# Kernel tuning notes

Measured on AMD Instinct MI355X. Metric: run time of the kernel, lower is better.

The kernel has to match this reference:

```python
import jax, jax.numpy as jnp
import numpy as np

D = 1024  # input_dim


def setup_inputs() -> dict:
    key = jax.random.key(0)
    ks = jax.random.split(key, 7)
    scale = 1.0 / np.sqrt(D)
    x = jax.random.normal(ks[0], (4, D, 2048), dtype=jnp.float32)
    Wq = jax.random.uniform(ks[1], (D, D), jnp.float32, -scale, scale)
    bq = jax.random.uniform(ks[2], (D,), jnp.float32, -scale, scale)
    Wk = jax.random.uniform(ks[3], (D, D), jnp.float32, -scale, scale)
    bk = jax.random.uniform(ks[4], (D,), jnp.float32, -scale, scale)
    Wv = jax.random.uniform(ks[5], (D, D), jnp.float32, -scale, scale)
    bv = jax.random.uniform(ks[6], (D,), jnp.float32, -scale, scale)
    return {"x": x, "Wq": Wq, "bq": bq, "Wk": Wk, "bk": bk, "Wv": Wv, "bv": bv}


def reference(x, Wq, bq, Wk, bk, Wv, bv):
    # x: [B, D, S] -> [B, S, D]
    xt = jnp.transpose(x, (0, 2, 1))
    # torch nn.Linear: y = x @ W^T + b
    q = jnp.einsum('bsd,ed->bse', xt, Wq) + bq
    k = jnp.einsum('bsd,ed->bse', xt, Wk) + bk
    v = jnp.einsum('bsd,ed->bse', xt, Wv) + bv
    scores = jnp.einsum('bse,bte->bst', q, k) / jnp.sqrt(jnp.float32(D))
    attn = jax.nn.softmax(scores, axis=2)
    out = jnp.einsum('bst,bte->bse', attn, v)  # [B, S, D]
    return out
```

## Files before the change

### kernel.cpp

```cpp
#include <hip/hip_runtime.h>
#include <stdint.h>

typedef unsigned short us16;
typedef unsigned short us8  __attribute__((ext_vector_type(8)));
typedef unsigned short us4v __attribute__((ext_vector_type(4)));
typedef __bf16         bf16x8 __attribute__((ext_vector_type(8)));
typedef float          f32x4  __attribute__((ext_vector_type(4)));

__device__ __forceinline__ us16 f2bf(float f) {
    union { float f; unsigned int u; } c; c.f = f;
    unsigned int u = (c.u + 0x7fffu + ((c.u >> 16) & 1u)) >> 16;
    return (us16)u;
}
__device__ __forceinline__ float bf2f(us16 h) {
    union { unsigned int u; float f; } c; c.u = ((unsigned int)h) << 16;
    return c.f;
}

__device__ __forceinline__ void async16(const us16* g, us16* l) {
    __builtin_amdgcn_global_load_lds(
        (const __attribute__((address_space(1))) unsigned int*)g,
        (__attribute__((address_space(3))) unsigned int*)l,
        16, 0, 0);
}

template <int EPI>
__device__ __forceinline__ void gemm_core(
        const us16* __restrict__ A, const us16* __restrict__ B,
        void* __restrict__ C, const float* __restrict__ bias,
        float* __restrict__ L,
        int M, int K, int x, int y, us16* lsA, us16* lsB) {
    const int m0 = x * 128, n0 = y * 128;
    const int tid = threadIdx.x;
    const int lane = tid & 63, wid = tid >> 6;
    const int l15 = lane & 15, quad = lane >> 4;
    const int wm = (wid & 1) * 64, wn = (wid >> 1) * 64;

    f32x4 acc[4][4] = {};

    const int srow = wid * 32 + (lane >> 3);
    const int sc8 = (lane & 7) ^ ((lane >> 3) & 7);
    const us16* Ap = A + (size_t)(m0 + srow) * K + sc8 * 8;
    const us16* Bp = B + (size_t)(n0 + srow) * K + sc8 * 8;
    us16* ldsAw = &lsA[(wid * 32) * 64];
    us16* ldsBw = &lsB[(wid * 32) * 64];

    for (int kb = 0; kb < K; kb += 64) {
        __syncthreads();
#pragma unroll
        for (int c = 0; c < 4; c++) {
            async16(Ap + kb + (size_t)(c * 8) * K, ldsAw + c * 8 * 64);
            async16(Bp + kb + (size_t)(c * 8) * K, ldsBw + c * 8 * 64);
        }
        __syncthreads();
#pragma unroll
        for (int ks = 0; ks < 2; ks++) {
            bf16x8 af[4], bfr[4];
#pragma unroll
            for (int i = 0; i < 4; i++) {
                const int ra = wm + i * 16 + l15;
                const int rb = wn + i * 16 + l15;
                const int pa = ((ks * 4 + quad) ^ (ra & 7)) * 8;
                const int pb = ((ks * 4 + quad) ^ (rb & 7)) * 8;
                af[i]  = *(const bf16x8*)(&lsA[ra * 64 + pa]);
                bfr[i] = *(const bf16x8*)(&lsB[rb * 64 + pb]);
            }
#pragma unroll
            for (int i = 0; i < 4; i++)
#pragma unroll
                for (int j = 0; j < 4; j++)
                    acc[i][j] = __builtin_amdgcn_mfma_f32_16x16x32_bf16(af[i], bfr[j], acc[i][j], 0, 0, 0);
        }
    }

    if (EPI == 2) {
        const float scale = 0.03125f;
        float rs[4] = {0.f, 0.f, 0.f, 0.f};
#pragma unroll
        for (int i = 0; i < 4; i++) {
            const int mb = m0 + wm + i * 16 + quad * 4;
#pragma unroll
            for (int j = 0; j < 4; j++) {
                const int n = n0 + wn + j * 16 + l15;
                f32x4 v = acc[i][j];
                const float e0 = __expf(v[0] * scale), e1 = __expf(v[1] * scale);
                const float e2 = __expf(v[2] * scale), e3 = __expf(v[3] * scale);
                rs[j] += (e0 + e1) + (e2 + e3);
                us4v st = { f2bf(e0), f2bf(e1), f2bf(e2), f2bf(e3) };
                *(us4v*)((us16*)C + (size_t)n * M + mb) = st;
            }
        }
#pragma unroll
        for (int j = 0; j < 4; j++) {
            rs[j] += __shfl_xor(rs[j], 16, 64);
            rs[j] += __shfl_xor(rs[j], 32, 64);
        }
        if (quad == 0) {
#pragma unroll
            for (int j = 0; j < 4; j++)
                atomicAdd(&L[n0 + wn + j * 16 + l15], rs[j]);
        }
        return;
    }

#pragma unroll
    for (int i = 0; i < 4; i++) {
        const int mb = m0 + wm + i * 16 + quad * 4;
        float b0 = 0.f, b1 = 0.f, b2 = 0.f, b3 = 0.f;
        if (EPI == 0) {
            float4 bv4 = *(const float4*)(bias + mb);
            b0 = bv4.x; b1 = bv4.y; b2 = bv4.z; b3 = bv4.w;
        }
#pragma unroll
        for (int j = 0; j < 4; j++) {
            const int n = n0 + wn + j * 16 + l15;
            f32x4 v = acc[i][j];
            if (EPI == 3) {
                const float inv = 1.0f / L[n];
                float4 st;
                st.x = v[0] * inv; st.y = v[1] * inv;
                st.z = v[2] * inv; st.w = v[3] * inv;
                *(float4*)((float*)C + (size_t)n * M + mb) = st;
            } else {
                const float bn = (EPI == 1) ? bias[n] : 0.0f;
                us4v st = { f2bf(v[0] + b0 + bn), f2bf(v[1] + b1 + bn),
                            f2bf(v[2] + b2 + bn), f2bf(v[3] + b3 + bn) };
                *(us4v*)((us16*)C + (size_t)n * M + mb) = st;
            }
        }
    }
}

__device__ __forceinline__ void strip_xy(int lin, int gy, int& x, int& y) {
    const int within = lin & (4 * gy - 1);
    x = (lin / (4 * gy)) * 4 + (within & 3);
    y = within >> 2;
}

__global__ __launch_bounds__(256)
void prep(const float* __restrict__ x, us16* __restrict__ xt,
          const float* __restrict__ wq, const float* __restrict__ wk,
          const float* __restrict__ wv, us16* __restrict__ wb) {
    __shared__ us16 tile[64 * 65];
    const int id = blockIdx.x;
    const int t = threadIdx.x;
    if (id < 2048) {
        const int s0 = (id & 31) * 64, d0 = ((id >> 5) & 15) * 64, b = id >> 9;
        const float* xp = x + ((size_t)b * 1024 + d0) * 2048 + s0;
        const int r = t >> 4, c4 = t & 15;
#pragma unroll
        for (int i = 0; i < 4; i++) {
            float4 v = *(const float4*)(xp + (size_t)(r + 16 * i) * 2048 + c4 * 4);
            const int d = r + 16 * i;
            tile[(c4 * 4 + 0) * 65 + d] = f2bf(v.x);
            tile[(c4 * 4 + 1) * 65 + d] = f2bf(v.y);
            tile[(c4 * 4 + 2) * 65 + d] = f2bf(v.z);
            tile[(c4 * 4 + 3) * 65 + d] = f2bf(v.w);
        }
        __syncthreads();
        us16* op = xt + ((size_t)b * 2048 + s0) * 1024 + d0;
#pragma unroll
        for (int i = 0; i < 2; i++) {
            const int u = t + 256 * i;
            const int s = u >> 3, c8 = u & 7;
            us8 o;
#pragma unroll
            for (int j = 0; j < 8; j++) o[j] = tile[s * 65 + c8 * 8 + j];
            *(us8*)(op + (size_t)s * 1024 + c8 * 8) = o;
        }
    } else {
        const int cid = id - 2048;
        const int mb = cid >> 10;
        const float* src = (mb == 0) ? wq : (mb == 1) ? wk : wv;
        const size_t off = ((size_t)(cid & 1023) * 256 + t) * 4;
        float4 v = *(const float4*)(src + off);
        us4v o = { f2bf(v.x), f2bf(v.y), f2bf(v.z), f2bf(v.w) };
        *(us4v*)(wb + (size_t)mb * 1048576 + off) = o;
    }
}

__global__ __launch_bounds__(256)
void qkv(const us16* __restrict__ Wb, const us16* __restrict__ XT,
         us16* __restrict__ Qb, us16* __restrict__ Kb, us16* __restrict__ VT,
         const float* __restrict__ bq, const float* __restrict__ bk,
         const float* __restrict__ bv) {
    __shared__ us16 lsA[128 * 64];
    __shared__ us16 lsB[128 * 64];
    const int id = blockIdx.x;
    const long long sXT = 2097152;
    if (id < 1024) {
        const int z = id >> 7, zz = z & 3;
        const bool isK = z >= 4;
        int x, y; strip_xy(id & 127, 16, x, y);
        const us16* A = Wb + (isK ? 1048576 : 0);
        const us16* B = XT + (size_t)zz * sXT;
        us16* C = (isK ? Kb : Qb) + (size_t)zz * sXT;
        gemm_core<0>(A, B, (void*)C, isK ? bk : bq, nullptr, 1024, 1024, x, y, lsA, lsB);
    } else {
        const int id2 = id - 1024;
        const int z = id2 >> 7;
        int x, y; strip_xy(id2 & 127, 8, x, y);
        const us16* A = XT + (size_t)z * sXT;
        us16* C = VT + (size_t)z * sXT;
        gemm_core<1>(A, Wb + 2097152, (void*)C, bv, nullptr, 2048, 1024, x, y, lsA, lsB);
    }
}

__global__ __launch_bounds__(256)
void scores_k(const us16* __restrict__ Kb, const us16* __restrict__ Qb,
              us16* __restrict__ Sb, float* __restrict__ L) {
    __shared__ us16 lsA[128 * 64];
    __shared__ us16 lsB[128 * 64];
    const long long sXT = 2097152, sSS = 4194304;
    const int z = blockIdx.z;
    int x, y; strip_xy(blockIdx.x + 16 * blockIdx.y, 16, x, y);
    gemm_core<2>(Kb + (size_t)z * sXT, Qb + (size_t)z * sXT,
                 (void*)(Sb + (size_t)z * sSS), nullptr, L + z * 2048,
                 2048, 1024, x, y, lsA, lsB);
}

__global__ __launch_bounds__(256)
void out_k(const us16* __restrict__ VT, const us16* __restrict__ Sb,
           float* __restrict__ L, float* __restrict__ out) {
    __shared__ us16 lsA[128 * 64];
    __shared__ us16 lsB[128 * 64];
    const long long sXT = 2097152, sSS = 4194304;
    const int z = blockIdx.z;
    int x, y; strip_xy(blockIdx.x + 8 * blockIdx.y, 16, x, y);
    gemm_core<3>(VT + (size_t)z * sXT, Sb + (size_t)z * sSS,
                 (void*)(out + (size_t)z * sXT), nullptr, L + z * 2048,
                 1024, 2048, x, y, lsA, lsB);
}

extern "C" void kernel_launch(void* const* d_in, const int* in_sizes, int n_in,
                              void* d_out, int out_size, void* d_ws, size_t ws_size,
                              hipStream_t stream) {
    const float* x  = (const float*)d_in[0];
    const float* Wq = (const float*)d_in[1];
    const float* bq = (const float*)d_in[2];
    const float* Wk = (const float*)d_in[3];
    const float* bk = (const float*)d_in[4];
    const float* Wv = (const float*)d_in[5];
    const float* bv = (const float*)d_in[6];
    float* out = (float*)d_out;
    char* ws = (char*)d_ws;

    const size_t SZ = 16777216;
    us16* Qb = (us16*)(ws);
    us16* Kb = (us16*)(ws + SZ);
    us16* VT = (us16*)(ws + 2 * SZ);
    us16* XT = (us16*)(ws + 3 * SZ);
    us16* Wb = (us16*)(ws + 4 * SZ);
    us16* Sb = (us16*)(ws + 3 * SZ);
    float* Lb = (float*)(ws + 5 * SZ);

    dim3 blk(256, 1, 1);

    hipMemsetAsync(Lb, 0, 4 * 2048 * sizeof(float), stream);
    prep<<<dim3(5120, 1, 1), blk, 0, stream>>>(x, XT, Wq, Wk, Wv, Wb);
    qkv<<<dim3(1536, 1, 1), blk, 0, stream>>>(Wb, XT, Qb, Kb, VT, bq, bk, bv);
    scores_k<<<dim3(16, 16, 4), blk, 0, stream>>>(Kb, Qb, Sb, Lb);
    out_k<<<dim3(8, 16, 4), blk, 0, stream>>>(VT, Sb, Lb, out);
}
```

Measured before the change: 252.4 us.

## Replace GEMM core with 4-stage async pipelined, larger-tile 512-thread kernel

Replaces the synchronous load-then-compute GEMM loop with a 4-buffer software pipeline that prefetches three K-slices of 32 ahead using async global-to-LDS loads. The code waits on them with explicit vmcnt counts and a single barrier per step. Tiles grow to 256x256 or 128x256 with 8 waves per block, and MFMA sections get raised priority. The aim is to hide global memory latency and increase reuse per block. The cost is much larger LDS use and fewer blocks, so occupancy and tail balance are at risk.

```diff
diff --git a/kernel.cpp b/kernel.cpp
--- a/kernel.cpp
+++ b/kernel.cpp
@@ -12,10 +12,6 @@
     unsigned int u = (c.u + 0x7fffu + ((c.u >> 16) & 1u)) >> 16;
     return (us16)u;
 }
-__device__ __forceinline__ float bf2f(us16 h) {
-    union { unsigned int u; float f; } c; c.u = ((unsigned int)h) << 16;
-    return c.f;
-}
 
 __device__ __forceinline__ void async16(const us16* g, us16* l) {
     __builtin_amdgcn_global_load_lds(
@@ -24,64 +20,113 @@
         16, 0, 0);
 }
 
-template <int EPI>
-__device__ __forceinline__ void gemm_core(
+template <int N> __device__ __forceinline__ void wait_vm() {
+    if constexpr (N == 8)      asm volatile("s_waitcnt vmcnt(8)" ::: "memory");
+    else if constexpr (N == 6) asm volatile("s_waitcnt vmcnt(6)" ::: "memory");
+    else if constexpr (N == 4) asm volatile("s_waitcnt vmcnt(4)" ::: "memory");
+    else if constexpr (N == 3) asm volatile("s_waitcnt vmcnt(3)" ::: "memory");
+    else                       asm volatile("s_waitcnt vmcnt(0)" ::: "memory");
+}
+
+template <int EPI, int MI, int NJ>
+__device__ __forceinline__ void gemm_pipe(
         const us16* __restrict__ A, const us16* __restrict__ B,
         void* __restrict__ C, const float* __restrict__ bias,
         float* __restrict__ L,
-        int M, int K, int x, int y, us16* lsA, us16* lsB) {
-    const int m0 = x * 128, n0 = y * 128;
-    const int tid = threadIdx.x;
+        int M, int K, int x, int y, us16* lds) {
+    constexpr int BM  = 32 * MI;
+    constexpr int BN  = 64 * NJ;
+    constexpr int IA  = BM / 128;
+    constexpr int IB  = BN / 128;
+    constexpr int EA  = BM * 32;
+    constexpr int BUF = EA + BN * 32;
+    constexpr int LD  = IA + IB;
+
+    const int tid  = threadIdx.x;
     const int lane = tid & 63, wid = tid >> 6;
-    const int l15 = lane & 15, quad = lane >> 4;
-    const int wm = (wid & 1) * 64, wn = (wid >> 1) * 64;
-
-    f32x4 acc[4][4] = {};
-
-    const int srow = wid * 32 + (lane >> 3);
-    const int sc8 = (lane & 7) ^ ((lane >> 3) & 7);
-    const us16* Ap = A + (size_t)(m0 + srow) * K + sc8 * 8;
-    const us16* Bp = B + (size_t)(n0 + srow) * K + sc8 * 8;
-    us16* ldsAw = &lsA[(wid * 32) * 64];
-    us16* ldsBw = &lsB[(wid * 32) * 64];
-
-    for (int kb = 0; kb < K; kb += 64) {
-        __syncthreads();
-#pragma unroll
-        for (int c = 0; c < 4; c++) {
-            async16(Ap + kb + (size_t)(c * 8) * K, ldsAw + c * 8 * 64);
-            async16(Bp + kb + (size_t)(c * 8) * K, ldsBw + c * 8 * 64);
-        }
-        __syncthreads();
-#pragma unroll
-        for (int ks = 0; ks < 2; ks++) {
-            bf16x8 af[4], bfr[4];
-#pragma unroll
-            for (int i = 0; i < 4; i++) {
-                const int ra = wm + i * 16 + l15;
-                const int rb = wn + i * 16 + l15;
-                const int pa = ((ks * 4 + quad) ^ (ra & 7)) * 8;
-                const int pb = ((ks * 4 + quad) ^ (rb & 7)) * 8;
-                af[i]  = *(const bf16x8*)(&lsA[ra * 64 + pa]);
-                bfr[i] = *(const bf16x8*)(&lsB[rb * 64 + pb]);
-            }
-#pragma unroll
-            for (int i = 0; i < 4; i++)
-#pragma unroll
-                for (int j = 0; j < 4; j++)
-                    acc[i][j] = __builtin_amdgcn_mfma_f32_16x16x32_bf16(af[i], bfr[j], acc[i][j], 0, 0, 0);
-        }
+    const int l15  = lane & 15, quad = lane >> 4;
+    const int wm   = wid >> 2, wn = wid & 3;
+    const int m0   = x * BM, n0 = y * BN;
+
+    const int gc8  = (((lane & 3) ^ ((lane >> 2) & 3) ^ ((lane >> 4) & 3))) * 8;
+    const int lsub = lane >> 2;
+
+    const us16* Ag[IA]; int Al[IA];
+#pragma unroll
+    for (int c = 0; c < IA; c++) {
+        const int r = wid * (16 * IA) + c * 16;
+        Ag[c] = A + (size_t)(m0 + r + lsub) * K + gc8;
+        Al[c] = r * 32;
+    }
+    const us16* Bg[IB]; int Bl[IB];
+#pragma unroll
+    for (int c = 0; c < IB; c++) {
+        const int r = wid * (16 * IB) + c * 16;
+        Bg[c] = B + (size_t)(n0 + r + lsub) * K + gc8;
+        Bl[c] = EA + r * 32;
+    }
+
+    const int NT  = K >> 5;
+    const int rc8    = ((quad ^ (l15 & 3) ^ ((l15 >> 2) & 3))) * 8;
+    const int raBase = wm * (MI * 16) + l15;
+    const int rbBase = wn * (NJ * 16) + l15;
+
+    f32x4 acc[MI][NJ] = {};
+
+#pragma unroll
+    for (int t = 0; t < 3; t++) {
+        us16* bp = lds + t * BUF;
+        const int ko = t * 32;
+#pragma unroll
+        for (int c = 0; c < IA; c++) async16(Ag[c] + ko, bp + Al[c]);
+#pragma unroll
+        for (int c = 0; c < IB; c++) async16(Bg[c] + ko, bp + Bl[c]);
+    }
+    wait_vm<2 * LD>();
+    __builtin_amdgcn_s_barrier();
+
+    for (int t = 0; t < NT; t++) {
+        if (t + 3 < NT) {
+            us16* bp = lds + ((t + 3) & 3) * BUF;
+            const int ko = (t + 3) * 32;
+#pragma unroll
+            for (int c = 0; c < IA; c++) async16(Ag[c] + ko, bp + Al[c]);
+#pragma unroll
+            for (int c = 0; c < IB; c++) async16(Bg[c] + ko, bp + Bl[c]);
+        }
+        const us16* bp = lds + (t & 3) * BUF;
+        bf16x8 af[MI], bfv[NJ];
+#pragma unroll
+        for (int i = 0; i < MI; i++)
+            af[i]  = *(const bf16x8*)(bp + (raBase + i * 16) * 32 + rc8);
+#pragma unroll
+        for (int j = 0; j < NJ; j++)
+            bfv[j] = *(const bf16x8*)(bp + EA + (rbBase + j * 16) * 32 + rc8);
+        __builtin_amdgcn_s_setprio(1);
+#pragma unroll
+        for (int i = 0; i < MI; i++)
+#pragma unroll
+            for (int j = 0; j < NJ; j++)
+                acc[i][j] = __builtin_amdgcn_mfma_f32_16x16x32_bf16(af[i], bfv[j], acc[i][j], 0, 0, 0);
+        __builtin_amdgcn_s_setprio(0);
+        if (t + 3 < NT)      wait_vm<2 * LD>();
+        else if (t + 2 < NT) wait_vm<LD>();
+        else if (t + 1 < NT) wait_vm<0>();
+        __builtin_amdgcn_sched_barrier(0);
+        __builtin_amdgcn_s_barrier();
     }
 
     if (EPI == 2) {
         const float scale = 0.03125f;
-        float rs[4] = {0.f, 0.f, 0.f, 0.f};
-#pragma unroll
-        for (int i = 0; i < 4; i++) {
-            const int mb = m0 + wm + i * 16 + quad * 4;
-#pragma unroll
-            for (int j = 0; j < 4; j++) {
-                const int n = n0 + wn + j * 16 + l15;
+        float rs[NJ];
+#pragma unroll
+        for (int j = 0; j < NJ; j++) rs[j] = 0.f;
+#pragma unroll
+        for (int i = 0; i < MI; i++) {
+            const int mb = m0 + wm * (MI * 16) + i * 16 + quad * 4;
+#pragma unroll
+            for (int j = 0; j < NJ; j++) {
+                const int n = n0 + wn * (NJ * 16) + j * 16 + l15;
                 f32x4 v = acc[i][j];
                 const float e0 = __expf(v[0] * scale), e1 = __expf(v[1] * scale);
                 const float e2 = __expf(v[2] * scale), e3 = __expf(v[3] * scale);
@@ -91,29 +136,29 @@
             }
         }
 #pragma unroll
-        for (int j = 0; j < 4; j++) {
+        for (int j = 0; j < NJ; j++) {
             rs[j] += __shfl_xor(rs[j], 16, 64);
             rs[j] += __shfl_xor(rs[j], 32, 64);
         }
         if (quad == 0) {
 #pragma unroll
-            for (int j = 0; j < 4; j++)
-                atomicAdd(&L[n0 + wn + j * 16 + l15], rs[j]);
+            for (int j = 0; j < NJ; j++)
+                atomicAdd(&L[n0 + wn * (NJ * 16) + j * 16 + l15], rs[j]);
         }
         return;
     }
 
 #pragma unroll
-    for (int i = 0; i < 4; i++) {
-        const int mb = m0 + wm + i * 16 + quad * 4;
+    for (int i = 0; i < MI; i++) {
+        const int mb = m0 + wm * (MI * 16) + i * 16 + quad * 4;
         float b0 = 0.f, b1 = 0.f, b2 = 0.f, b3 = 0.f;
         if (EPI == 0) {
             float4 bv4 = *(const float4*)(bias + mb);
             b0 = bv4.x; b1 = bv4.y; b2 = bv4.z; b3 = bv4.w;
         }
 #pragma unroll
-        for (int j = 0; j < 4; j++) {
-            const int n = n0 + wn + j * 16 + l15;
+        for (int j = 0; j < NJ; j++) {
+            const int n = n0 + wn * (NJ * 16) + j * 16 + l15;
             f32x4 v = acc[i][j];
             if (EPI == 3) {
                 const float inv = 1.0f / L[n];
@@ -179,57 +224,55 @@
     }
 }
 
-__global__ __launch_bounds__(256)
+__global__ __launch_bounds__(512)
 void qkv(const us16* __restrict__ Wb, const us16* __restrict__ XT,
          us16* __restrict__ Qb, us16* __restrict__ Kb, us16* __restrict__ VT,
          const float* __restrict__ bq, const float* __restrict__ bk,
          const float* __restrict__ bv) {
-    __shared__ us16 lsA[128 * 64];
-    __shared__ us16 lsB[128 * 64];
+    __shared__ __align__(16) us16 lds[65536];
     const int id = blockIdx.x;
     const long long sXT = 2097152;
-    if (id < 1024) {
-        const int z = id >> 7, zz = z & 3;
+    if (id < 256) {
+        const int z = id >> 5, zz = z & 3;
         const bool isK = z >= 4;
-        int x, y; strip_xy(id & 127, 16, x, y);
+        int x, y; strip_xy(id & 31, 8, x, y);
         const us16* A = Wb + (isK ? 1048576 : 0);
         const us16* B = XT + (size_t)zz * sXT;
         us16* C = (isK ? Kb : Qb) + (size_t)zz * sXT;
-        gemm_core<0>(A, B, (void*)C, isK ? bk : bq, nullptr, 1024, 1024, x, y, lsA, lsB);
+        gemm_pipe<0, 8, 4>(A, B, (void*)C, isK ? bk : bq, nullptr,
+                           1024, 1024, x, y, lds);
     } else {
-        const int id2 = id - 1024;
-        const int z = id2 >> 7;
-        int x, y; strip_xy(id2 & 127, 8, x, y);
-        const us16* A = XT + (size_t)z * sXT;
-        us16* C = VT + (size_t)z * sXT;
-        gemm_core<1>(A, Wb + 2097152, (void*)C, bv, nullptr, 2048, 1024, x, y, lsA, lsB);
-    }
-}
-
-__global__ __launch_bounds__(256)
+        const int id2 = id - 256;
+        const int z = id2 >> 6;
+        int x, y; strip_xy(id2 & 63, 4, x, y);
+        gemm_pipe<1, 4, 4>(XT + (size_t)z * sXT, Wb + 2097152,
+                           (void*)(VT + (size_t)z * sXT), bv, nullptr,
+                           2048, 1024, x, y, lds);
+    }
+}
+
+__global__ __launch_bounds__(512)
 void scores_k(const us16* __restrict__ Kb, const us16* __restrict__ Qb,
               us16* __restrict__ Sb, float* __restrict__ L) {
-    __shared__ us16 lsA[128 * 64];
-    __shared__ us16 lsB[128 * 64];
+    __shared__ __align__(16) us16 lds[65536];
     const long long sXT = 2097152, sSS = 4194304;
     const int z = blockIdx.z;
-    int x, y; strip_xy(blockIdx.x + 16 * blockIdx.y, 16, x, y);
-    gemm_core<2>(Kb + (size_t)z * sXT, Qb + (size_t)z * sXT,
-                 (void*)(Sb + (size_t)z * sSS), nullptr, L + z * 2048,
-                 2048, 1024, x, y, lsA, lsB);
-}
-
-__global__ __launch_bounds__(256)
+    int x, y; strip_xy(blockIdx.x + 8 * blockIdx.y, 8, x, y);
+    gemm_pipe<2, 8, 4>(Kb + (size_t)z * sXT, Qb + (size_t)z * sXT,
+                       (void*)(Sb + (size_t)z * sSS), nullptr, L + z * 2048,
+                       2048, 1024, x, y, lds);
+}
+
+__global__ __launch_bounds__(512)
 void out_k(const us16* __restrict__ VT, const us16* __restrict__ Sb,
            float* __restrict__ L, float* __restrict__ out) {
-    __shared__ us16 lsA[128 * 64];
-    __shared__ us16 lsB[128 * 64];
+    __shared__ __align__(16) us16 lds[49152];
     const long long sXT = 2097152, sSS = 4194304;
     const int z = blockIdx.z;
-    int x, y; strip_xy(blockIdx.x + 8 * blockIdx.y, 16, x, y);
-    gemm_core<3>(VT + (size_t)z * sXT, Sb + (size_t)z * sSS,
-                 (void*)(out + (size_t)z * sXT), nullptr, L + z * 2048,
-                 1024, 2048, x, y, lsA, lsB);
+    int x, y; strip_xy(blockIdx.x + 8 * blockIdx.y, 8, x, y);
+    gemm_pipe<3, 4, 4>(VT + (size_t)z * sXT, Sb + (size_t)z * sSS,
+                       (void*)(out + (size_t)z * sXT), nullptr, L + z * 2048,
+                       1024, 2048, x, y, lds);
 }
 
 extern "C" void kernel_launch(void* const* d_in, const int* in_sizes, int n_in,
@@ -254,11 +297,9 @@
     us16* Sb = (us16*)(ws + 3 * SZ);
     float* Lb = (float*)(ws + 5 * SZ);
 
-    dim3 blk(256, 1, 1);
-
     hipMemsetAsync(Lb, 0, 4 * 2048 * sizeof(float), stream);
-    prep<<<dim3(5120, 1, 1), blk, 0, stream>>>(x, XT, Wq, Wk, Wv, Wb);
-    qkv<<<dim3(1536, 1, 1), blk, 0, stream>>>(Wb, XT, Qb, Kb, VT, bq, bk, bv);
-    scores_k<<<dim3(16, 16, 4), blk, 0, stream>>>(Kb, Qb, Sb, Lb);
-    out_k<<<dim3(8, 16, 4), blk, 0, stream>>>(VT, Sb, Lb, out);
-}
+    prep<<<dim3(5120, 1, 1), dim3(256, 1, 1), 0, stream>>>(x, XT, Wq, Wk, Wv, Wb);
+    qkv<<<dim3(512, 1, 1), dim3(512, 1, 1), 0, stream>>>(Wb, XT, Qb, Kb, VT, bq, bk, bv);
+    scores_k<<<dim3(8, 8, 4), dim3(512, 1, 1), 0, stream>>>(Kb, Qb, Sb, Lb);
+    out_k<<<dim3(8, 8, 4), dim3(512, 1, 1), 0, stream>>>(VT, Sb, Lb, out);
+}
```

Result: faster. 244.5 us (-3.1%).
